# Kernel optimization log

Hardware: AMD Instinct MI355X
Metric: run time of the kernel (lower is better)

## Reference

```python
import jax, jax.numpy as jnp
import numpy as np

NEAR_THRESHOLD = 0.3
NUM_HEADING_BIN = 12
NUM_SIZE_CLUSTER = 18
NUM_CLASS = 18
BN_EPS = 1e-5


def setup_inputs() -> dict:
    key = jax.random.key(0)
    ks = jax.random.split(key, 16)
    B, K, C, KG = 256, 256, 128, 64
    OUT = 3 + NUM_HEADING_BIN * 2 + NUM_SIZE_CLUSTER * 4 + NUM_CLASS  # 117
    return {
        "xyz": jax.random.normal(ks[0], (B, K, 3), jnp.float32),
        "features": jax.random.normal(ks[1], (B, C, K), jnp.float32),
        "rn_feature": jax.random.normal(ks[2], (B, C, K), jnp.float32),
        "gt_center": jax.random.normal(ks[3], (B, KG, 3), jnp.float32),
        "objectness_pred": jax.random.randint(ks[4], (B, K), 0, 2, jnp.int64),
        "W1": jax.random.normal(ks[5], (C, 2 * C), jnp.float32) * 0.05,
        "b1": jax.random.normal(ks[6], (C,), jnp.float32) * 0.05,
        "g1": jnp.ones((C,), jnp.float32),
        "be1": jnp.zeros((C,), jnp.float32),
        "W2": jax.random.normal(ks[7], (C, C), jnp.float32) * 0.05,
        "b2": jax.random.normal(ks[8], (C,), jnp.float32) * 0.05,
        "g2": jnp.ones((C,), jnp.float32),
        "be2": jnp.zeros((C,), jnp.float32),
        "W3": jax.random.normal(ks[9], (OUT, C), jnp.float32) * 0.05,
        "b3": jax.random.normal(ks[10], (OUT,), jnp.float32) * 0.05,
        "mean_size": jax.random.uniform(ks[11], (NUM_SIZE_CLUSTER, 3), jnp.float32),
    }


def nn_distance_min(a, b):
    # a: (B,K,3), b: (B,KG,3) -> min squared distance from each a to b
    d = jnp.sum((a[:, :, None, :] - b[:, None, :, :]) ** 2, axis=-1)  # (B,K,KG)
    return jnp.min(d, axis=2)


def get_index(pred):
    # vectorized stream compaction: per row, indices where pred==1 packed first,
    # remaining slots keep arange identity (matches torch get_index semantics).
    B, K = pred.shape
    idx = jnp.arange(K, dtype=jnp.int64)
    key = jnp.where(pred == 1, idx[None, :], idx[None, :] + K)
    srt = jnp.sort(key, axis=1)
    num = jnp.sum(pred, axis=1)  # (B,)
    idx_obj = jnp.where(idx[None, :] < num[:, None], srt, idx[None, :])
    return idx_obj, num


def bn_relu(x, g, b):
    # training-mode BatchNorm1d over (B, C, K): stats over batch+points
    mn = jnp.mean(x, axis=(0, 2), keepdims=True)
    vr = jnp.var(x, axis=(0, 2), keepdims=True)
    xn = (x - mn) * jax.lax.rsqrt(vr + BN_EPS)
    return jax.nn.relu(xn * g[None, :, None] + b[None, :, None])


def reference(xyz, features, rn_feature, gt_center, objectness_pred,
              W1, b1, g1, be1, W2, b2, g2, be2, W3, b3, mean_size):
    B, K, _ = xyz.shape
    # objectness labeling via nn_distance
    dist1 = nn_distance_min(xyz, gt_center)
    euclid = jnp.sqrt(dist1 + 1e-6)
    objectness_label = (euclid < NEAR_THRESHOLD).astype(jnp.int64)
    # stream compaction on predicted objectness
    idx_obj, sum_1 = get_index(objectness_pred)
    # conv1d(k=1) / BN / ReLU head
    feat = jnp.concatenate([features, rn_feature], axis=1)  # (B, 256, K)
    net = bn_relu(jnp.einsum('oc,bck->bok', W1, feat) + b1[None, :, None], g1, be1)
    net = bn_relu(jnp.einsum('oc,bck->bok', W2, net) + b2[None, :, None], g2, be2)
    net = jnp.einsum('oc,bck->bok', W3, net) + b3[None, :, None]  # (B,117,K)
    # decode_scores_pred
    t = jnp.transpose(net, (0, 2, 1))  # (B,K,117)
    nh, ns = NUM_HEADING_BIN, NUM_SIZE_CLUSTER
    center = xyz + t[:, :, 0:3]
    hs = t[:, :, 3:3 + nh]
    hrn = t[:, :, 3 + nh:3 + 2 * nh]
    hr = hrn * (np.pi / nh)
    ss = t[:, :, 3 + 2 * nh:3 + 2 * nh + ns]
    srn = t[:, :, 3 + 2 * nh + ns:3 + 2 * nh + 4 * ns].reshape(B, K, ns, 3)
    sr = srn * mean_size[None, None, :, :]
    sem = t[:, :, 3 + 2 * nh + 4 * ns:]
    out = jnp.concatenate(
        [center, hs, hrn, hr, ss,
         srn.reshape(B, K, ns * 3), sr.reshape(B, K, ns * 3), sem], axis=-1)
    return out, idx_obj, sum_1, objectness_label
```

## Files before the change

### kernel.cpp

```cpp
#include <hip/hip_runtime.h>
#include <hip/hip_bf16.h>
#include <math.h>

#define B_  256
#define K_  256
#define C_  128
#define KG_ 64
#define O3_ 117
#define OD_ 183

typedef unsigned int  u32;
typedef unsigned short u16;
typedef __bf16 bf16_t;
typedef bf16_t bf16x8 __attribute__((ext_vector_type(8)));
typedef float  f32x4  __attribute__((ext_vector_type(4)));

__device__ __forceinline__ float bflo(u32 u){ return __uint_as_float(u << 16); }
__device__ __forceinline__ float bfhi(u32 u){ return __uint_as_float(u & 0xffff0000u); }
__device__ __forceinline__ u16 f2bf(float f){
    __hip_bfloat16 h = __float2bfloat16(f);
    return __builtin_bit_cast(u16, h);
}
__device__ __forceinline__ int swz(int row, int byteInRow){
    return row * 256 + (byteInRow ^ (((row >> 1) & 7) << 4));
}

__global__ __launch_bounds__(256) void misc_kernel(const float* __restrict__ xyz,
                                                   const float* __restrict__ gtc,
                                                   const int*   __restrict__ pred,
                                                   const float* __restrict__ W1,
                                                   const float* __restrict__ W2,
                                                   const float* __restrict__ W3,
                                                   u16* __restrict__ W1bf,
                                                   u16* __restrict__ W2bf,
                                                   u16* __restrict__ W3bf,
                                                   float* __restrict__ label,
                                                   float* __restrict__ idxo,
                                                   float* __restrict__ sum1)
{
    const int blk = blockIdx.x, t = threadIdx.x;
    if (blk < 256) {
        __shared__ float g[KG_ * 3];
        const int b = blk;
        if (t < KG_ * 3) g[t] = gtc[(size_t)b * KG_ * 3 + t];
        __syncthreads();
        const size_t pidx = (size_t)(b * K_ + t);
        float x = xyz[pidx * 3 + 0];
        float y = xyz[pidx * 3 + 1];
        float z = xyz[pidx * 3 + 2];
        float dmin = 1e30f;
#pragma unroll 8
        for (int j = 0; j < KG_; ++j) {
            float dx = x - g[j * 3 + 0];
            float dy = y - g[j * 3 + 1];
            float dz = z - g[j * 3 + 2];
            float d  = dx * dx + dy * dy + dz * dz;
            dmin = fminf(dmin, d);
        }
        float e = sqrtf(dmin + 1e-6f);
        label[pidx] = (e < 0.3f) ? 1.0f : 0.0f;
    } else if (blk < 512) {
        const int b = blk - 256;
        const int p = (pred[b * K_ + t] == 1) ? 1 : 0;
        __shared__ int sd[K_];
        sd[t] = p;
        __syncthreads();
        for (int off = 1; off < K_; off <<= 1) {
            int v = (t >= off) ? sd[t - off] : 0;
            __syncthreads();
            sd[t] += v;
            __syncthreads();
        }
        const int incl = sd[t];
        const int num  = sd[K_ - 1];
        if (t >= num) idxo[b * K_ + t] = (float)t;
        if (p)        idxo[b * K_ + (incl - p)] = (float)t;
        if (t == 0)   sum1[b] = (float)num;
    } else {
        int idx = (blk - 512) * 256 + t;
        if (idx < 32768) {
            W1bf[idx] = f2bf(W1[idx]);
        } else if (idx < 49152) {
            int j = idx - 32768;
            W2bf[j] = f2bf(W2[j]);
        } else {
            int j = idx - 49152;
            int row = j >> 7, col = j & 127;
            W3bf[j] = (row < O3_) ? f2bf(W3[row * C_ + col]) : (u16)0;
        }
    }
}

__device__ __forceinline__ void epilogue_store(char* smem, const f32x4 acc[2][8],
                                               const float* __restrict__ bias,
                                               u16* __restrict__ outp, float* __restrict__ part,
                                               int pb, int t, int w, int lr, int lg)
{
    float* SP = (float*)(smem + 40960);
    float* SQ = (float*)(smem + 49152);
#pragma unroll
    for (int n = 0; n < 8; ++n) {
        int o = n * 16 + lr;
        float bvn = bias[o];
        float s = 0.f, q = 0.f;
#pragma unroll
        for (int m = 0; m < 2; ++m) {
            float v0 = acc[m][n][0] + bvn;
            float v1 = acc[m][n][1] + bvn;
            float v2 = acc[m][n][2] + bvn;
            float v3 = acc[m][n][3] + bvn;
            s += (v0 + v1) + (v2 + v3);
            q = fmaf(v0, v0, q); q = fmaf(v1, v1, q);
            q = fmaf(v2, v2, q); q = fmaf(v3, v3, q);
            uint2 pk;
            pk.x = (u32)f2bf(v0) | ((u32)f2bf(v1) << 16);
            pk.y = (u32)f2bf(v2) | ((u32)f2bf(v3) << 16);
            *(uint2*)(smem + o * 264 + (w * 32 + m * 16 + lg * 4) * 2) = pk;
        }
        SP[(w * 4 + lg) * 128 + o] = s;
        SQ[(w * 4 + lg) * 128 + o] = q;
    }
    __syncthreads();
    u16* dst = outp + (size_t)pb * 16384;
#pragma unroll
    for (int j = 0; j < 8; ++j) {
        int i = t + j * 256;
        int c = i >> 4, col = i & 15;
        uint4 v = *(const uint4*)(smem + c * 264 + col * 16);
        *(uint4*)(dst + c * 128 + col * 8) = v;
    }
    if (t < 128) {
        float s = 0.f, q = 0.f;
#pragma unroll
        for (int i = 0; i < 16; ++i) { s += SP[i * 128 + t]; q += SQ[i * 128 + t]; }
        part[pb * 256 + t] = s;
        part[pb * 256 + 128 + t] = q;
    }
}

__device__ __forceinline__ void stage_bn(char* smem, const u16* __restrict__ net,
                                         const float* __restrict__ sc,
                                         const float* __restrict__ sh, int pb, int t)
{
    const u16* tile = net + (size_t)pb * 16384;
    const int q = t & 15, cb = t >> 4;
#pragma unroll
    for (int j = 0; j < 2; ++j) {
        int c0 = j * 64 + cb * 4;
        u32 R[4][4];
#pragma unroll
        for (int i2 = 0; i2 < 4; ++i2) {
            uint4 v = *(const uint4*)(tile + (c0 + i2) * 128 + q * 8);
            R[i2][0] = v.x; R[i2][1] = v.y; R[i2][2] = v.z; R[i2][3] = v.w;
        }
        float ss[4], tt[4];
#pragma unroll
        for (int i2 = 0; i2 < 4; ++i2) { ss[i2] = sc[c0 + i2]; tt[i2] = sh[c0 + i2]; }
#pragma unroll
        for (int p = 0; p < 8; ++p) {
            int wi = p >> 1;
            float f0, f1, f2, f3;
            if (p & 1) {
                f0 = bfhi(R[0][wi]); f1 = bfhi(R[1][wi]);
                f2 = bfhi(R[2][wi]); f3 = bfhi(R[3][wi]);
            } else {
                f0 = bflo(R[0][wi]); f1 = bflo(R[1][wi]);
                f2 = bflo(R[2][wi]); f3 = bflo(R[3][wi]);
            }
            f0 = fmaxf(0.f, fmaf(f0, ss[0], tt[0]));
            f1 = fmaxf(0.f, fmaf(f1, ss[1], tt[1]));
            f2 = fmaxf(0.f, fmaf(f2, ss[2], tt[2]));
            f3 = fmaxf(0.f, fmaf(f3, ss[3], tt[3]));
            uint2 pk;
            pk.x = (u32)f2bf(f0) | ((u32)f2bf(f1) << 16);
            pk.y = (u32)f2bf(f2) | ((u32)f2bf(f3) << 16);
            int row = q * 8 + p;
            *(uint2*)(smem + swz(row, c0 * 2)) = pk;
        }
    }
}

__device__ __forceinline__ void stage_w128(char* smem, const u16* __restrict__ Wbf, int t)
{
    int c8 = (t & 15) * 8;
#pragma unroll
    for (int rr = 0; rr < 8; ++rr) {
        int row = (t >> 4) + rr * 16;
        uint4 v = *(const uint4*)(Wbf + (size_t)row * 128 + c8);
        *(uint4*)(smem + 32768 + swz(row, c8 * 2)) = v;
    }
}

__device__ __forceinline__ void compute_tile(char* smem, f32x4 acc[2][8], int w, int lr, int lg)
{
#pragma unroll
    for (int ks = 0; ks < 4; ++ks) {
        bf16x8 a[2], bfr[8];
#pragma unroll
        for (int m = 0; m < 2; ++m) {
            int row = w * 32 + m * 16 + lr;
            a[m] = *(const bf16x8*)(smem + swz(row, ks * 64 + lg * 16));
        }
#pragma unroll
        for (int n = 0; n < 8; ++n) {
            int row = n * 16 + lr;
            bfr[n] = *(const bf16x8*)(smem + 32768 + swz(row, ks * 64 + lg * 16));
        }
#pragma unroll
        for (int m = 0; m < 2; ++m)
#pragma unroll
            for (int n = 0; n < 8; ++n)
                acc[m][n] = __builtin_amdgcn_mfma_f32_16x16x32_bf16(a[m], bfr[n], acc[m][n], 0, 0, 0);
    }
}

__global__ __launch_bounds__(256) void gemm1_kernel(const float* __restrict__ fa,
                                                    const float* __restrict__ fb,
                                                    const u16* __restrict__ Wbf,
                                                    const float* __restrict__ bias,
                                                    u16* __restrict__ outp,
                                                    float* __restrict__ part)
{
    __shared__ __align__(16) char smem[65536];
    const int t   = threadIdx.x;
    const int pb  = blockIdx.x;
    const int pt0 = pb * 128;
    const int bb  = pt0 >> 8;
    const int k0  = pt0 & 255;
    const int w   = t >> 6, l = t & 63;
    const int lr  = l & 15, lg = l >> 4;

    f32x4 acc[2][8] = {};

    for (int ph = 0; ph < 2; ++ph) {
        if (ph) __syncthreads();
        const float* src = (ph == 0) ? fa : fb;
        {
            const int q  = t & 31;
            const int cb = t >> 5;
#pragma unroll
            for (int j = 0; j < 4; ++j) {
                int cq = cb + j * 8;
                float4 r0 = *(const float4*)(src + ((size_t)(bb*C_ + cq*4 + 0))*K_ + k0 + q*4);
                float4 r1 = *(const float4*)(src + ((size_t)(bb*C_ + cq*4 + 1))*K_ + k0 + q*4);
                float4 r2 = *(const float4*)(src + ((size_t)(bb*C_ + cq*4 + 2))*K_ + k0 + q*4);
                float4 r3 = *(const float4*)(src + ((size_t)(bb*C_ + cq*4 + 3))*K_ + k0 + q*4);
                const float* p0 = (const float*)&r0;
                const float* p1 = (const float*)&r1;
                const float* p2 = (const float*)&r2;
                const float* p3 = (const float*)&r3;
#pragma unroll
                for (int p = 0; p < 4; ++p) {
                    int row = q * 4 + p;
                    uint2 uv;
                    uv.x = (u32)f2bf(p0[p]) | ((u32)f2bf(p1[p]) << 16);
                    uv.y = (u32)f2bf(p2[p]) | ((u32)f2bf(p3[p]) << 16);
                    *(uint2*)(smem + swz(row, cq * 8)) = uv;
                }
            }
        }
        {
            int c8 = (t & 15) * 8;
#pragma unroll
            for (int rr = 0; rr < 8; ++rr) {
                int row = (t >> 4) + rr * 16;
                uint4 v = *(const uint4*)(Wbf + (size_t)row * 256 + ph * 128 + c8);
                *(uint4*)(smem + 32768 + swz(row, c8 * 2)) = v;
            }
        }
        __syncthreads();
        compute_tile(smem, acc, w, lr, lg);
    }
    __syncthreads();
    epilogue_store(smem, acc, bias, outp, part, pb, t, w, lr, lg);
}

__global__ __launch_bounds__(64) void finalize_kernel(const float* __restrict__ part,
                                                      const float* __restrict__ g,
                                                      const float* __restrict__ be,
                                                      float* __restrict__ sc,
                                                      float* __restrict__ sh)
{
    const int c = blockIdx.x, l = threadIdx.x;
    float s = 0.f, q = 0.f;
#pragma unroll
    for (int i = 0; i < 8; ++i) {
        int pb = l + i * 64;
        s += part[pb * 256 + c];
        q += part[pb * 256 + 128 + c];
    }
#pragma unroll
    for (int off = 32; off > 0; off >>= 1) {
        s += __shfl_down(s, off);
        q += __shfl_down(q, off);
    }
    if (l == 0) {
        const float inv = 1.0f / 65536.0f;
        float mean = s * inv;
        float var  = q * inv - mean * mean;
        float scv  = g[c] * rsqrtf(var + 1e-5f);
        sc[c] = scv;
        sh[c] = be[c] - mean * scv;
    }
}

__global__ __launch_bounds__(256) void gemm2_kernel(const u16* __restrict__ net,
                                                    const float* __restrict__ sc,
                                                    const float* __restrict__ sh,
                                                    const u16* __restrict__ Wbf,
                                                    const float* __restrict__ bias,
                                                    u16* __restrict__ outp,
                                                    float* __restrict__ part)
{
    __shared__ __align__(16) char smem[65536];
    const int t  = threadIdx.x;
    const int pb = blockIdx.x;
    const int w  = t >> 6, l = t & 63;
    const int lr = l & 15, lg = l >> 4;

    stage_bn(smem, net, sc, sh, pb, t);
    stage_w128(smem, Wbf, t);
    __syncthreads();

    f32x4 acc[2][8] = {};
    compute_tile(smem, acc, w, lr, lg);
    __syncthreads();
    epilogue_store(smem, acc, bias, outp, part, pb, t, w, lr, lg);
}

__global__ __launch_bounds__(256) void gemm3_kernel(const u16* __restrict__ net,
                                                    const float* __restrict__ sc,
                                                    const float* __restrict__ sh,
                                                    const u16* __restrict__ Wbf,
                                                    const float* __restrict__ bias,
                                                    const float* __restrict__ xyz,
                                                    const float* __restrict__ msize,
                                                    float* __restrict__ out)
{
    __shared__ __align__(16) char smem[65536];
    const int t   = threadIdx.x;
    const int pb  = blockIdx.x;
    const int pt0 = pb * 128;
    const int w   = t >> 6, l = t & 63;
    const int lr  = l & 15, lg = l >> 4;

    stage_bn(smem, net, sc, sh, pb, t);
    stage_w128(smem, Wbf, t);
    __syncthreads();

    f32x4 acc[2][8] = {};
    compute_tile(smem, acc, w, lr, lg);

    const float PI12 = 0.26179938779914946f;
    for (int s = 0; s < 2; ++s) {
        __syncthreads();
        if ((w >> 1) == s) {
            float* Of = (float*)smem + (w & 1) * (32 * 184);
#pragma unroll
            for (int n = 0; n < 8; ++n) {
                int o = n * 16 + lr;
                if (o < O3_) {
                    float bvn = bias[o];
                    float msv = (o >= 45 && o < 99) ? msize[o - 45] : 0.f;
#pragma unroll
                    for (int m = 0; m < 2; ++m)
#pragma unroll
                        for (int r = 0; r < 4; ++r) {
                            int pl = m * 16 + lg * 4 + r;
                            float v = acc[m][n][r] + bvn;
                            float* row = Of + pl * 184;
                            if (o < 3) {
                                int gp = pt0 + w * 32 + pl;
                                row[o] = v + xyz[(size_t)gp * 3 + o];
                            } else if (o < 15) {
                                row[o] = v;
                            } else if (o < 27) {
                                row[o] = v; row[o + 12] = v * PI12;
                            } else if (o < 45) {
                                row[o + 12] = v;
                            } else if (o < 99) {
                                row[o + 12] = v; row[o + 66] = v * msv;
                            } else {
                                row[o + 66] = v;
                            }
                        }
                }
            }
        }
        __syncthreads();
        float* Ob = out + (size_t)(pt0 + s * 64) * OD_;
        const float* Sf = (const float*)smem;
        for (int i = t; i < 64 * OD_; i += 256) {
            int pl  = (int)(((u32)i * 91680u) >> 24);
            int col = i - pl * 183;
            Ob[i] = Sf[(pl >> 5) * (32 * 184) + (pl & 31) * 184 + col];
        }
    }
}

extern "C" void kernel_launch(void* const* d_in, const int* in_sizes, int n_in,
                              void* d_out, int out_size, void* d_ws, size_t ws_size,
                              hipStream_t stream)
{
    const float* xyz      = (const float*)d_in[0];
    const float* features = (const float*)d_in[1];
    const float* rn       = (const float*)d_in[2];
    const float* gtc      = (const float*)d_in[3];
    const int*   pred     = (const int*)d_in[4];
    const float* W1  = (const float*)d_in[5];
    const float* b1  = (const float*)d_in[6];
    const float* g1  = (const float*)d_in[7];
    const float* be1 = (const float*)d_in[8];
    const float* W2  = (const float*)d_in[9];
    const float* b2  = (const float*)d_in[10];
    const float* g2  = (const float*)d_in[11];
    const float* be2 = (const float*)d_in[12];
    const float* W3  = (const float*)d_in[13];
    const float* b3  = (const float*)d_in[14];
    const float* ms  = (const float*)d_in[15];

    float* out = (float*)d_out;
    const size_t OFF_IDX = (size_t)B_ * K_ * OD_;
    const size_t OFF_SUM = OFF_IDX + (size_t)B_ * K_;
    const size_t OFF_LAB = OFF_SUM + B_;

    char* ws = (char*)d_ws;
    u16*  net1 = (u16*)ws;
    u16*  net2 = (u16*)(ws + 16777216);
    u16*  W1bf = (u16*)(ws + 33554432);
    u16*  W2bf = (u16*)(ws + 33619968);
    u16*  W3bf = (u16*)(ws + 33652736);
    float* part1 = (float*)(ws + 33685504);
    float* part2 = (float*)(ws + 34209792);
    float* coef  = (float*)(ws + 34734080);
    float* sc1 = coef;        float* sh1 = coef + 128;
    float* sc2 = coef + 256;  float* sh2 = coef + 384;

    misc_kernel<<<768, 256, 0, stream>>>(xyz, gtc, pred, W1, W2, W3,
                                         W1bf, W2bf, W3bf,
                                         out + OFF_LAB, out + OFF_IDX, out + OFF_SUM);

    gemm1_kernel<<<512, 256, 0, stream>>>(features, rn, W1bf, b1, net1, part1);
    finalize_kernel<<<128, 64, 0, stream>>>(part1, g1, be1, sc1, sh1);

    gemm2_kernel<<<512, 256, 0, stream>>>(net1, sc1, sh1, W2bf, b2, net2, part2);
    finalize_kernel<<<128, 64, 0, stream>>>(part2, g2, be2, sc2, sh2);

    gemm3_kernel<<<512, 256, 0, stream>>>(net2, sc2, sh2, W3bf, b3, xyz, ms, out);
}
```

Measured before the change: 183.9 us.

## Fuse misc work into GEMM1 and fold BN finalize into consumer GEMMs

Cuts the launch sequence from six kernels to three. The nearest-distance label and compaction work moves into the first GEMM kernel as extra blocks. Weights are converted from fp32 to bf16 inside each GEMM block instead of in a separate pre-pass. The separate BN finalize kernels are removed: every block of GEMM2 and GEMM3 redundantly reduces all 512 partial sums to compute the scale and shift. This trades launch gaps and serialization for redundant per-block reduction traffic (512 blocks × 512 KB of part reads, largely served from cache) and extra per-block weight conversion.

```diff
diff --git a/kernel.cpp b/kernel.cpp
--- a/kernel.cpp
+++ b/kernel.cpp
@@ -9,6 +9,11 @@
 #define O3_ 117
 #define OD_ 183
 
+#define A_OFF    0
+#define W_OFF    32768
+#define RED_OFF  0
+#define SCSH_OFF 4096
+
 typedef unsigned int  u32;
 typedef unsigned short u16;
 typedef __bf16 bf16_t;
@@ -25,76 +30,81 @@
     return row * 256 + (byteInRow ^ (((row >> 1) & 7) << 4));
 }
 
-__global__ __launch_bounds__(256) void misc_kernel(const float* __restrict__ xyz,
-                                                   const float* __restrict__ gtc,
-                                                   const int*   __restrict__ pred,
-                                                   const float* __restrict__ W1,
-                                                   const float* __restrict__ W2,
-                                                   const float* __restrict__ W3,
-                                                   u16* __restrict__ W1bf,
-                                                   u16* __restrict__ W2bf,
-                                                   u16* __restrict__ W3bf,
-                                                   float* __restrict__ label,
-                                                   float* __restrict__ idxo,
-                                                   float* __restrict__ sum1)
-{
-    const int blk = blockIdx.x, t = threadIdx.x;
-    if (blk < 256) {
-        __shared__ float g[KG_ * 3];
-        const int b = blk;
-        if (t < KG_ * 3) g[t] = gtc[(size_t)b * KG_ * 3 + t];
-        __syncthreads();
-        const size_t pidx = (size_t)(b * K_ + t);
-        float x = xyz[pidx * 3 + 0];
-        float y = xyz[pidx * 3 + 1];
-        float z = xyz[pidx * 3 + 2];
-        float dmin = 1e30f;
-#pragma unroll 8
-        for (int j = 0; j < KG_; ++j) {
-            float dx = x - g[j * 3 + 0];
-            float dy = y - g[j * 3 + 1];
-            float dz = z - g[j * 3 + 2];
-            float d  = dx * dx + dy * dy + dz * dz;
-            dmin = fminf(dmin, d);
-        }
-        float e = sqrtf(dmin + 1e-6f);
-        label[pidx] = (e < 0.3f) ? 1.0f : 0.0f;
-    } else if (blk < 512) {
-        const int b = blk - 256;
-        const int p = (pred[b * K_ + t] == 1) ? 1 : 0;
-        __shared__ int sd[K_];
-        sd[t] = p;
-        __syncthreads();
-        for (int off = 1; off < K_; off <<= 1) {
-            int v = (t >= off) ? sd[t - off] : 0;
-            __syncthreads();
-            sd[t] += v;
-            __syncthreads();
-        }
-        const int incl = sd[t];
-        const int num  = sd[K_ - 1];
-        if (t >= num) idxo[b * K_ + t] = (float)t;
-        if (p)        idxo[b * K_ + (incl - p)] = (float)t;
-        if (t == 0)   sum1[b] = (float)num;
-    } else {
-        int idx = (blk - 512) * 256 + t;
-        if (idx < 32768) {
-            W1bf[idx] = f2bf(W1[idx]);
-        } else if (idx < 49152) {
-            int j = idx - 32768;
-            W2bf[j] = f2bf(W2[j]);
-        } else {
-            int j = idx - 49152;
-            int row = j >> 7, col = j & 127;
-            W3bf[j] = (row < O3_) ? f2bf(W3[row * C_ + col]) : (u16)0;
-        }
+__device__ __forceinline__ void stageA_f32(char* smem, const float* __restrict__ src,
+                                           int bb, int k0, int t)
+{
+    const int q  = t & 31;
+    const int cb = t >> 5;
+#pragma unroll
+    for (int j = 0; j < 4; ++j) {
+        int cq = cb + j * 8;
+        float4 r0 = *(const float4*)(src + ((size_t)(bb*C_ + cq*4 + 0))*K_ + k0 + q*4);
+        float4 r1 = *(const float4*)(src + ((size_t)(bb*C_ + cq*4 + 1))*K_ + k0 + q*4);
+        float4 r2 = *(const float4*)(src + ((size_t)(bb*C_ + cq*4 + 2))*K_ + k0 + q*4);
+        float4 r3 = *(const float4*)(src + ((size_t)(bb*C_ + cq*4 + 3))*K_ + k0 + q*4);
+        const float* p0 = (const float*)&r0;
+        const float* p1 = (const float*)&r1;
+        const float* p2 = (const float*)&r2;
+        const float* p3 = (const float*)&r3;
+#pragma unroll
+        for (int p = 0; p < 4; ++p) {
+            int row = q * 4 + p;
+            uint2 uv;
+            uv.x = (u32)f2bf(p0[p]) | ((u32)f2bf(p1[p]) << 16);
+            uv.y = (u32)f2bf(p2[p]) | ((u32)f2bf(p3[p]) << 16);
+            *(uint2*)(smem + A_OFF + swz(row, cq * 8)) = uv;
+        }
+    }
+}
+
+__device__ __forceinline__ void stageW_f32(char* smem, const float* __restrict__ W,
+                                           int ldw, int colOff, int rowLimit, int t)
+{
+    int c8 = (t & 15) * 8;
+#pragma unroll
+    for (int rr = 0; rr < 8; ++rr) {
+        int row = (t >> 4) + rr * 16;
+        uint4 q2 = {0, 0, 0, 0};
+        if (row < rowLimit) {
+            float4 v0 = *(const float4*)(W + (size_t)row * ldw + colOff + c8);
+            float4 v1 = *(const float4*)(W + (size_t)row * ldw + colOff + c8 + 4);
+            q2.x = (u32)f2bf(v0.x) | ((u32)f2bf(v0.y) << 16);
+            q2.y = (u32)f2bf(v0.z) | ((u32)f2bf(v0.w) << 16);
+            q2.z = (u32)f2bf(v1.x) | ((u32)f2bf(v1.y) << 16);
+            q2.w = (u32)f2bf(v1.z) | ((u32)f2bf(v1.w) << 16);
+        }
+        *(uint4*)(smem + W_OFF + swz(row, c8 * 2)) = q2;
+    }
+}
+
+__device__ __forceinline__ void compute_tile(const char* smem, f32x4 acc[2][8],
+                                             int w, int lr, int lg)
+{
+#pragma unroll
+    for (int ks = 0; ks < 4; ++ks) {
+        bf16x8 a[2], bfr[8];
+#pragma unroll
+        for (int m = 0; m < 2; ++m) {
+            int row = w * 32 + m * 16 + lr;
+            a[m] = *(const bf16x8*)(smem + A_OFF + swz(row, ks * 64 + lg * 16));
+        }
+#pragma unroll
+        for (int n = 0; n < 8; ++n) {
+            int row = n * 16 + lr;
+            bfr[n] = *(const bf16x8*)(smem + W_OFF + swz(row, ks * 64 + lg * 16));
+        }
+#pragma unroll
+        for (int m = 0; m < 2; ++m)
+#pragma unroll
+            for (int n = 0; n < 8; ++n)
+                acc[m][n] = __builtin_amdgcn_mfma_f32_16x16x32_bf16(a[m], bfr[n], acc[m][n], 0, 0, 0);
     }
 }
 
 __device__ __forceinline__ void epilogue_store(char* smem, const f32x4 acc[2][8],
                                                const float* __restrict__ bias,
                                                u16* __restrict__ outp, float* __restrict__ part,
-                                               int pb, int t, int w, int lr, int lg)
+                                               int tb, int t, int w, int lr, int lg)
 {
     float* SP = (float*)(smem + 40960);
     float* SQ = (float*)(smem + 49152);
@@ -121,7 +131,7 @@
         SQ[(w * 4 + lg) * 128 + o] = q;
     }
     __syncthreads();
-    u16* dst = outp + (size_t)pb * 16384;
+    u16* dst = outp + (size_t)tb * 16384;
 #pragma unroll
     for (int j = 0; j < 8; ++j) {
         int i = t + j * 256;
@@ -133,16 +143,66 @@
         float s = 0.f, q = 0.f;
 #pragma unroll
         for (int i = 0; i < 16; ++i) { s += SP[i * 128 + t]; q += SQ[i * 128 + t]; }
-        part[pb * 256 + t] = s;
-        part[pb * 256 + 128 + t] = q;
-    }
-}
-
-__device__ __forceinline__ void stage_bn(char* smem, const u16* __restrict__ net,
-                                         const float* __restrict__ sc,
-                                         const float* __restrict__ sh, int pb, int t)
-{
-    const u16* tile = net + (size_t)pb * 16384;
+        part[tb * 256 + t] = s;
+        part[tb * 256 + 128 + t] = q;
+    }
+}
+
+__device__ __forceinline__ void reduce_finalize(char* smem, const float* __restrict__ part,
+                                                const float* __restrict__ g,
+                                                const float* __restrict__ be, int t)
+{
+    float4* redf4 = (float4*)(smem + RED_OFF);
+    const int q4 = t & 63, slice = t >> 6;
+    float4 v = {0.f, 0.f, 0.f, 0.f};
+    const float* base = part + q4 * 4;
+#pragma unroll 8
+    for (int i = 0; i < 128; ++i) {
+        float4 p = *(const float4*)(base + (size_t)(slice * 128 + i) * 256);
+        v.x += p.x; v.y += p.y; v.z += p.z; v.w += p.w;
+    }
+    redf4[slice * 64 + q4] = v;
+    __syncthreads();
+    float* scsh = (float*)(smem + SCSH_OFF);
+    if (t < 64) {
+        float4 a = redf4[t], b = redf4[64 + t], c = redf4[128 + t], d = redf4[192 + t];
+        float4 s;
+        s.x = (a.x + b.x) + (c.x + d.x);
+        s.y = (a.y + b.y) + (c.y + d.y);
+        s.z = (a.z + b.z) + (c.z + d.z);
+        s.w = (a.w + b.w) + (c.w + d.w);
+        *(float4*)(scsh + t * 4) = s;
+    }
+    __syncthreads();
+    if (t < 128) {
+        const float inv = 1.0f / 65536.0f;
+        float mean = scsh[t] * inv;
+        float var  = scsh[128 + t] * inv - mean * mean;
+        float sv   = g[t] * rsqrtf(var + 1e-5f);
+        float shv  = be[t] - mean * sv;
+        scsh[t] = sv;
+        scsh[128 + t] = shv;
+    }
+}
+
+__device__ __forceinline__ void load_coefs(const char* smem, float ss[2][4], float tt[2][4], int t)
+{
+    const float* scsh = (const float*)(smem + SCSH_OFF);
+    const int cb = t >> 4;
+#pragma unroll
+    for (int j = 0; j < 2; ++j) {
+        int c0 = j * 64 + cb * 4;
+#pragma unroll
+        for (int i2 = 0; i2 < 4; ++i2) {
+            ss[j][i2] = scsh[c0 + i2];
+            tt[j][i2] = scsh[128 + c0 + i2];
+        }
+    }
+}
+
+__device__ __forceinline__ void stage_bn_reg(char* smem, const u16* __restrict__ tile,
+                                             const float ss[2][4], const float tt[2][4], int t)
+{
     const int q = t & 15, cb = t >> 4;
 #pragma unroll
     for (int j = 0; j < 2; ++j) {
@@ -150,12 +210,9 @@
         u32 R[4][4];
 #pragma unroll
         for (int i2 = 0; i2 < 4; ++i2) {
-            uint4 v = *(const uint4*)(tile + (c0 + i2) * 128 + q * 8);
+            uint4 v = *(const uint4*)(tile + (size_t)(c0 + i2) * 128 + q * 8);
             R[i2][0] = v.x; R[i2][1] = v.y; R[i2][2] = v.z; R[i2][3] = v.w;
         }
-        float ss[4], tt[4];
-#pragma unroll
-        for (int i2 = 0; i2 < 4; ++i2) { ss[i2] = sc[c0 + i2]; tt[i2] = sh[c0 + i2]; }
 #pragma unroll
         for (int p = 0; p < 8; ++p) {
             int wi = p >> 1;
@@ -167,188 +224,148 @@
                 f0 = bflo(R[0][wi]); f1 = bflo(R[1][wi]);
                 f2 = bflo(R[2][wi]); f3 = bflo(R[3][wi]);
             }
-            f0 = fmaxf(0.f, fmaf(f0, ss[0], tt[0]));
-            f1 = fmaxf(0.f, fmaf(f1, ss[1], tt[1]));
-            f2 = fmaxf(0.f, fmaf(f2, ss[2], tt[2]));
-            f3 = fmaxf(0.f, fmaf(f3, ss[3], tt[3]));
+            f0 = fmaxf(0.f, fmaf(f0, ss[j][0], tt[j][0]));
+            f1 = fmaxf(0.f, fmaf(f1, ss[j][1], tt[j][1]));
+            f2 = fmaxf(0.f, fmaf(f2, ss[j][2], tt[j][2]));
+            f3 = fmaxf(0.f, fmaf(f3, ss[j][3], tt[j][3]));
             uint2 pk;
             pk.x = (u32)f2bf(f0) | ((u32)f2bf(f1) << 16);
             pk.y = (u32)f2bf(f2) | ((u32)f2bf(f3) << 16);
-            int row = q * 8 + p;
-            *(uint2*)(smem + swz(row, c0 * 2)) = pk;
-        }
-    }
-}
-
-__device__ __forceinline__ void stage_w128(char* smem, const u16* __restrict__ Wbf, int t)
-{
-    int c8 = (t & 15) * 8;
-#pragma unroll
-    for (int rr = 0; rr < 8; ++rr) {
-        int row = (t >> 4) + rr * 16;
-        uint4 v = *(const uint4*)(Wbf + (size_t)row * 128 + c8);
-        *(uint4*)(smem + 32768 + swz(row, c8 * 2)) = v;
-    }
-}
-
-__device__ __forceinline__ void compute_tile(char* smem, f32x4 acc[2][8], int w, int lr, int lg)
-{
-#pragma unroll
-    for (int ks = 0; ks < 4; ++ks) {
-        bf16x8 a[2], bfr[8];
-#pragma unroll
-        for (int m = 0; m < 2; ++m) {
-            int row = w * 32 + m * 16 + lr;
-            a[m] = *(const bf16x8*)(smem + swz(row, ks * 64 + lg * 16));
-        }
-#pragma unroll
-        for (int n = 0; n < 8; ++n) {
-            int row = n * 16 + lr;
-            bfr[n] = *(const bf16x8*)(smem + 32768 + swz(row, ks * 64 + lg * 16));
-        }
-#pragma unroll
-        for (int m = 0; m < 2; ++m)
-#pragma unroll
-            for (int n = 0; n < 8; ++n)
-                acc[m][n] = __builtin_amdgcn_mfma_f32_16x16x32_bf16(a[m], bfr[n], acc[m][n], 0, 0, 0);
-    }
-}
-
-__global__ __launch_bounds__(256) void gemm1_kernel(const float* __restrict__ fa,
+            *(uint2*)(smem + A_OFF + swz(q * 8 + p, c0 * 2)) = pk;
+        }
+    }
+}
+
+__global__ __launch_bounds__(256, 2) void k1_kernel(const float* __restrict__ fa,
                                                     const float* __restrict__ fb,
-                                                    const u16* __restrict__ Wbf,
-                                                    const float* __restrict__ bias,
-                                                    u16* __restrict__ outp,
-                                                    float* __restrict__ part)
+                                                    const float* __restrict__ W1,
+                                                    const float* __restrict__ b1,
+                                                    const float* __restrict__ xyz,
+                                                    const float* __restrict__ gtc,
+                                                    const int*   __restrict__ pred,
+                                                    u16* __restrict__ act1,
+                                                    float* __restrict__ part1,
+                                                    float* __restrict__ label,
+                                                    float* __restrict__ idxo,
+                                                    float* __restrict__ sum1)
 {
     __shared__ __align__(16) char smem[65536];
-    const int t   = threadIdx.x;
-    const int pb  = blockIdx.x;
-    const int pt0 = pb * 128;
-    const int bb  = pt0 >> 8;
-    const int k0  = pt0 & 255;
-    const int w   = t >> 6, l = t & 63;
-    const int lr  = l & 15, lg = l >> 4;
-
-    f32x4 acc[2][8] = {};
-
-    for (int ph = 0; ph < 2; ++ph) {
-        if (ph) __syncthreads();
-        const float* src = (ph == 0) ? fa : fb;
-        {
-            const int q  = t & 31;
-            const int cb = t >> 5;
-#pragma unroll
-            for (int j = 0; j < 4; ++j) {
-                int cq = cb + j * 8;
-                float4 r0 = *(const float4*)(src + ((size_t)(bb*C_ + cq*4 + 0))*K_ + k0 + q*4);
-                float4 r1 = *(const float4*)(src + ((size_t)(bb*C_ + cq*4 + 1))*K_ + k0 + q*4);
-                float4 r2 = *(const float4*)(src + ((size_t)(bb*C_ + cq*4 + 2))*K_ + k0 + q*4);
-                float4 r3 = *(const float4*)(src + ((size_t)(bb*C_ + cq*4 + 3))*K_ + k0 + q*4);
-                const float* p0 = (const float*)&r0;
-                const float* p1 = (const float*)&r1;
-                const float* p2 = (const float*)&r2;
-                const float* p3 = (const float*)&r3;
-#pragma unroll
-                for (int p = 0; p < 4; ++p) {
-                    int row = q * 4 + p;
-                    uint2 uv;
-                    uv.x = (u32)f2bf(p0[p]) | ((u32)f2bf(p1[p]) << 16);
-                    uv.y = (u32)f2bf(p2[p]) | ((u32)f2bf(p3[p]) << 16);
-                    *(uint2*)(smem + swz(row, cq * 8)) = uv;
-                }
-            }
-        }
-        {
-            int c8 = (t & 15) * 8;
-#pragma unroll
-            for (int rr = 0; rr < 8; ++rr) {
-                int row = (t >> 4) + rr * 16;
-                uint4 v = *(const uint4*)(Wbf + (size_t)row * 256 + ph * 128 + c8);
-                *(uint4*)(smem + 32768 + swz(row, c8 * 2)) = v;
-            }
-        }
+    const int blk = blockIdx.x, t = threadIdx.x;
+
+    if (blk < 512) {
+        const int pb = blk;
+        const int bb = pb >> 1;
+        const int k0 = (pb & 1) << 7;
+        const int w  = t >> 6, l = t & 63;
+        const int lr = l & 15, lg = l >> 4;
+
+        f32x4 acc[2][8] = {};
+        stageA_f32(smem, fa, bb, k0, t);
+        stageW_f32(smem, W1, 256, 0, 128, t);
         __syncthreads();
         compute_tile(smem, acc, w, lr, lg);
-    }
-    __syncthreads();
-    epilogue_store(smem, acc, bias, outp, part, pb, t, w, lr, lg);
-}
-
-__global__ __launch_bounds__(64) void finalize_kernel(const float* __restrict__ part,
-                                                      const float* __restrict__ g,
-                                                      const float* __restrict__ be,
-                                                      float* __restrict__ sc,
-                                                      float* __restrict__ sh)
-{
-    const int c = blockIdx.x, l = threadIdx.x;
-    float s = 0.f, q = 0.f;
-#pragma unroll
-    for (int i = 0; i < 8; ++i) {
-        int pb = l + i * 64;
-        s += part[pb * 256 + c];
-        q += part[pb * 256 + 128 + c];
-    }
-#pragma unroll
-    for (int off = 32; off > 0; off >>= 1) {
-        s += __shfl_down(s, off);
-        q += __shfl_down(q, off);
-    }
-    if (l == 0) {
-        const float inv = 1.0f / 65536.0f;
-        float mean = s * inv;
-        float var  = q * inv - mean * mean;
-        float scv  = g[c] * rsqrtf(var + 1e-5f);
-        sc[c] = scv;
-        sh[c] = be[c] - mean * scv;
-    }
-}
-
-__global__ __launch_bounds__(256) void gemm2_kernel(const u16* __restrict__ net,
-                                                    const float* __restrict__ sc,
-                                                    const float* __restrict__ sh,
-                                                    const u16* __restrict__ Wbf,
-                                                    const float* __restrict__ bias,
-                                                    u16* __restrict__ outp,
-                                                    float* __restrict__ part)
+        __syncthreads();
+        stageA_f32(smem, fb, bb, k0, t);
+        stageW_f32(smem, W1, 256, 128, 128, t);
+        __syncthreads();
+        compute_tile(smem, acc, w, lr, lg);
+        __syncthreads();
+        epilogue_store(smem, acc, b1, act1, part1, pb, t, w, lr, lg);
+    } else if (blk < 768) {
+        float* gg = (float*)smem;
+        const int b = blk - 512;
+        if (t < KG_ * 3) gg[t] = gtc[(size_t)b * KG_ * 3 + t];
+        __syncthreads();
+        const size_t pidx = (size_t)(b * K_ + t);
+        float x = xyz[pidx * 3 + 0];
+        float y = xyz[pidx * 3 + 1];
+        float z = xyz[pidx * 3 + 2];
+        float dmin = 1e30f;
+#pragma unroll 8
+        for (int j = 0; j < KG_; ++j) {
+            float dx = x - gg[j * 3 + 0];
+            float dy = y - gg[j * 3 + 1];
+            float dz = z - gg[j * 3 + 2];
+            float d  = dx * dx + dy * dy + dz * dz;
+            dmin = fminf(dmin, d);
+        }
+        float e = sqrtf(dmin + 1e-6f);
+        label[pidx] = (e < 0.3f) ? 1.0f : 0.0f;
+    } else {
+        int* sd = (int*)smem;
+        const int b = blk - 768;
+        const int p = (pred[b * K_ + t] == 1) ? 1 : 0;
+        sd[t] = p;
+        __syncthreads();
+        for (int off = 1; off < K_; off <<= 1) {
+            int v = (t >= off) ? sd[t - off] : 0;
+            __syncthreads();
+            sd[t] += v;
+            __syncthreads();
+        }
+        const int incl = sd[t];
+        const int num  = sd[K_ - 1];
+        if (t >= num) idxo[b * K_ + t] = (float)t;
+        if (p)        idxo[b * K_ + (incl - p)] = (float)t;
+        if (t == 0)   sum1[b] = (float)num;
+    }
+}
+
+__global__ __launch_bounds__(256, 2) void k2_kernel(const u16* __restrict__ act1,
+                                                    const float* __restrict__ part1,
+                                                    const float* __restrict__ g1,
+                                                    const float* __restrict__ be1,
+                                                    const float* __restrict__ W2,
+                                                    const float* __restrict__ b2,
+                                                    u16* __restrict__ act2,
+                                                    float* __restrict__ part2)
 {
     __shared__ __align__(16) char smem[65536];
-    const int t  = threadIdx.x;
-    const int pb = blockIdx.x;
+    const int pb = blockIdx.x, t = threadIdx.x;
     const int w  = t >> 6, l = t & 63;
     const int lr = l & 15, lg = l >> 4;
 
-    stage_bn(smem, net, sc, sh, pb, t);
-    stage_w128(smem, Wbf, t);
+    reduce_finalize(smem, part1, g1, be1, t);
+    __syncthreads();
+    float ss[2][4], tt[2][4];
+    load_coefs(smem, ss, tt, t);
     __syncthreads();
 
     f32x4 acc[2][8] = {};
+    stage_bn_reg(smem, act1 + (size_t)pb * 16384, ss, tt, t);
+    stageW_f32(smem, W2, 128, 0, 128, t);
+    __syncthreads();
     compute_tile(smem, acc, w, lr, lg);
     __syncthreads();
-    epilogue_store(smem, acc, bias, outp, part, pb, t, w, lr, lg);
-}
-
-__global__ __launch_bounds__(256) void gemm3_kernel(const u16* __restrict__ net,
-                                                    const float* __restrict__ sc,
-                                                    const float* __restrict__ sh,
-                                                    const u16* __restrict__ Wbf,
-                                                    const float* __restrict__ bias,
+    epilogue_store(smem, acc, b2, act2, part2, pb, t, w, lr, lg);
+}
+
+__global__ __launch_bounds__(256, 2) void k3_kernel(const u16* __restrict__ act2,
+                                                    const float* __restrict__ part2,
+                                                    const float* __restrict__ g2,
+                                                    const float* __restrict__ be2,
+                                                    const float* __restrict__ W3,
+                                                    const float* __restrict__ b3,
                                                     const float* __restrict__ xyz,
                                                     const float* __restrict__ msize,
                                                     float* __restrict__ out)
 {
     __shared__ __align__(16) char smem[65536];
-    const int t   = threadIdx.x;
-    const int pb  = blockIdx.x;
+    const int pb = blockIdx.x, t = threadIdx.x;
     const int pt0 = pb * 128;
-    const int w   = t >> 6, l = t & 63;
-    const int lr  = l & 15, lg = l >> 4;
-
-    stage_bn(smem, net, sc, sh, pb, t);
-    stage_w128(smem, Wbf, t);
+    const int w  = t >> 6, l = t & 63;
+    const int lr = l & 15, lg = l >> 4;
+
+    reduce_finalize(smem, part2, g2, be2, t);
+    __syncthreads();
+    float ss[2][4], tt[2][4];
+    load_coefs(smem, ss, tt, t);
     __syncthreads();
 
     f32x4 acc[2][8] = {};
+    stage_bn_reg(smem, act2 + (size_t)pb * 16384, ss, tt, t);
+    stageW_f32(smem, W3, 128, 0, O3_, t);
+    __syncthreads();
     compute_tile(smem, acc, w, lr, lg);
 
     const float PI12 = 0.26179938779914946f;
@@ -360,7 +377,7 @@
             for (int n = 0; n < 8; ++n) {
                 int o = n * 16 + lr;
                 if (o < O3_) {
-                    float bvn = bias[o];
+                    float bvn = b3[o];
                     float msv = (o >= 45 && o < 99) ? msize[o - 45] : 0.f;
 #pragma unroll
                     for (int m = 0; m < 2; ++m)
@@ -425,26 +442,14 @@
     const size_t OFF_LAB = OFF_SUM + B_;
 
     char* ws = (char*)d_ws;
-    u16*  net1 = (u16*)ws;
-    u16*  net2 = (u16*)(ws + 16777216);
-    u16*  W1bf = (u16*)(ws + 33554432);
-    u16*  W2bf = (u16*)(ws + 33619968);
-    u16*  W3bf = (u16*)(ws + 33652736);
-    float* part1 = (float*)(ws + 33685504);
-    float* part2 = (float*)(ws + 34209792);
-    float* coef  = (float*)(ws + 34734080);
-    float* sc1 = coef;        float* sh1 = coef + 128;
-    float* sc2 = coef + 256;  float* sh2 = coef + 384;
-
-    misc_kernel<<<768, 256, 0, stream>>>(xyz, gtc, pred, W1, W2, W3,
-                                         W1bf, W2bf, W3bf,
-                                         out + OFF_LAB, out + OFF_IDX, out + OFF_SUM);
-
-    gemm1_kernel<<<512, 256, 0, stream>>>(features, rn, W1bf, b1, net1, part1);
-    finalize_kernel<<<128, 64, 0, stream>>>(part1, g1, be1, sc1, sh1);
-
-    gemm2_kernel<<<512, 256, 0, stream>>>(net1, sc1, sh1, W2bf, b2, net2, part2);
-    finalize_kernel<<<128, 64, 0, stream>>>(part2, g2, be2, sc2, sh2);
-
-    gemm3_kernel<<<512, 256, 0, stream>>>(net2, sc2, sh2, W3bf, b3, xyz, ms, out);
-}
+    u16*  act1  = (u16*)ws;
+    u16*  act2  = (u16*)(ws + 16777216);
+    float* part1 = (float*)(ws + 33554432);
+    float* part2 = (float*)(ws + 34078720);
+
+    k1_kernel<<<1024, 256, 0, stream>>>(features, rn, W1, b1, xyz, gtc, pred,
+                                        act1, part1,
+                                        out + OFF_LAB, out + OFF_IDX, out + OFF_SUM);
+    k2_kernel<<<512, 256, 0, stream>>>(act1, part1, g1, be1, W2, b2, act2, part2);
+    k3_kernel<<<512, 256, 0, stream>>>(act2, part2, g2, be2, W3, b3, xyz, ms, out);
+}
```

After: 194.8 us. 1.06x slower.
